# Kernel tuning notes

Hardware: AMD Instinct MI355X
Metric: run time of the kernel (lower is better)

## Reference

```python
import jax, jax.numpy as jnp
import numpy as np

D_MODEL = 2048
NUM_HEADS = 16
D_K = D_MODEL // NUM_HEADS
THETA = 10000.0
MAX_SEQ_LEN = 2048
GPT_INIT_STD = 0.02


def setup_inputs() -> dict:
    key = jax.random.key(0)
    ks = jax.random.split(key, 5)
    B, T = 4, 2048
    x = jax.random.normal(ks[0], (B, T, D_MODEL), dtype=jnp.float32)
    token_positions = jnp.arange(T, dtype=jnp.int64 if jax.config.jax_enable_x64 else jnp.int32)[None, :]
    Wq = jax.random.normal(ks[1], (D_MODEL, D_MODEL), dtype=jnp.float32) * GPT_INIT_STD
    Wk = jax.random.normal(ks[2], (D_MODEL, D_MODEL), dtype=jnp.float32) * GPT_INIT_STD
    Wv = jax.random.normal(ks[3], (D_MODEL, D_MODEL), dtype=jnp.float32) * GPT_INIT_STD
    Wo = jax.random.normal(ks[4], (D_MODEL, D_MODEL), dtype=jnp.float32) * GPT_INIT_STD
    return {"x": x, "token_positions": token_positions, "Wq": Wq, "Wk": Wk, "Wv": Wv, "Wo": Wo}


def _rope_tables(dtype):
    # angles[p, j] = p * theta^(-2j/d_k), j in [0, d_k/2)
    j = jnp.arange(D_K // 2, dtype=jnp.float32)
    inv_freq = THETA ** (-2.0 * j / float(D_K))
    pos = jnp.arange(MAX_SEQ_LEN, dtype=jnp.float32)[:, None]
    angles = pos * inv_freq[None, :]
    return jnp.cos(angles).astype(dtype), jnp.sin(angles).astype(dtype)


def _apply_rope(t, cos_pos, sin_pos):
    # t: (b, h, s, d); cos/sin: (1, s, d/2) -> broadcast over (b, h)
    even = t[..., 0::2]
    odd = t[..., 1::2]
    c = cos_pos[:, None, :, :]  # (1,1,s,d/2)
    s = sin_pos[:, None, :, :]
    rot_even = even * c - odd * s
    rot_odd = even * s + odd * c
    out = jnp.stack([rot_even, rot_odd], axis=-1)  # (b,h,s,d/2,2)
    return out.reshape(t.shape)


def reference(x, token_positions, Wq, Wk, Wv, Wo):
    B, T, D = x.shape
    H, d = NUM_HEADS, D_K
    q = (x @ Wq.T).reshape(B, T, H, d).transpose(0, 2, 1, 3)  # (b,h,t,d)
    k = (x @ Wk.T).reshape(B, T, H, d).transpose(0, 2, 1, 3)
    v = (x @ Wv.T).reshape(B, T, H, d).transpose(0, 2, 1, 3)

    cos_tab, sin_tab = _rope_tables(x.dtype)
    cos_pos = cos_tab[token_positions]  # (1, t, d/2)
    sin_pos = sin_tab[token_positions]
    q = _apply_rope(q, cos_pos, sin_pos)
    k = _apply_rope(k, cos_pos, sin_pos)

    # token_positions is strictly increasing and attention_mask is None,
    # so build_attention_mask returns None -> unmasked eager attention.
    scale = float(d) ** -0.5
    scores = jnp.einsum('bhtd,bhsd->bhts', q, k) * scale
    attn = jax.nn.softmax(scores.astype(jnp.float32), axis=-1).astype(q.dtype)
    out = jnp.einsum('bhts,bhsd->bhtd', attn, v)  # (b,h,t,d)
    out = out.transpose(0, 2, 1, 3).reshape(B, T, D)  # (b,t,h*d)
    return out @ Wo.T
```

## Files before the change

kernel.cpp:

```cpp
#include <hip/hip_runtime.h>
#include <hip/hip_bf16.h>
#include <hip/hip_fp16.h>
#include <math.h>

#define TSEQ   2048
#define DMODEL 2048
#define NHEAD  16
#define DHEAD  128
#define NBATCH 4
#define MROWS  (NBATCH*TSEQ)

typedef __attribute__((ext_vector_type(8))) short v8s;
typedef __attribute__((ext_vector_type(4))) float v4f;
typedef __attribute__((ext_vector_type(16))) float v16f;

#if __has_builtin(__builtin_amdgcn_exp2f)
#define EXP2(x) __builtin_amdgcn_exp2f(x)
#else
#define EXP2(x) __expf((x) * 0.6931471805599453f)
#endif

__device__ __forceinline__ unsigned short f2b(float f) {
  __hip_bfloat16 h = __float2bfloat16(f);
  return *reinterpret_cast<unsigned short*>(&h);
}
__device__ __forceinline__ float b2f(unsigned int u) {
  unsigned short us = (unsigned short)u;
  __hip_bfloat16 h = *reinterpret_cast<__hip_bfloat16*>(&us);
  return __bfloat162float(h);
}
__device__ __forceinline__ unsigned int cvtpk(float lo, float hi) {
  unsigned int r;
  asm("v_cvt_pk_bf16_f32 %0, %1, %2" : "=v"(r) : "v"(lo), "v"(hi));
  return r;
}
__device__ __forceinline__ void gload_lds16(const unsigned short* g, unsigned short* l) {
  __builtin_amdgcn_global_load_lds(
      (const __attribute__((address_space(1))) unsigned int*)g,
      (__attribute__((address_space(3))) unsigned int*)l, 16, 0, 0);
}

__global__ void prep_kernel(const float* __restrict__ x,  const float* __restrict__ Wq,
                            const float* __restrict__ Wk, const float* __restrict__ Wv,
                            const float* __restrict__ Wo, const int* __restrict__ pos,
                            unsigned short* __restrict__ xb,  unsigned short* __restrict__ wqb,
                            unsigned short* __restrict__ wkb, unsigned short* __restrict__ wvb,
                            unsigned short* __restrict__ wob,
                            unsigned int* __restrict__ ropeT) {
  const int blk = blockIdx.x, tid = threadIdx.x;
  if (blk < 32768) {
    const float* in; unsigned short* out; int lb;
    if      (blk < 16384) { in = x;  out = xb;  lb = blk; }
    else if (blk < 20480) { in = Wq; out = wqb; lb = blk - 16384; }
    else if (blk < 24576) { in = Wk; out = wkb; lb = blk - 20480; }
    else if (blk < 28672) { in = Wv; out = wvb; lb = blk - 24576; }
    else                  { in = Wo; out = wob; lb = blk - 28672; }
    int i = lb * 256 + tid;
    float4 v = reinterpret_cast<const float4*>(in)[i];
    ushort4 o;
    o.x = f2b(v.x); o.y = f2b(v.y); o.z = f2b(v.z); o.w = f2b(v.w);
    reinterpret_cast<ushort4*>(out)[i] = o;
  } else {
    int idx = (blk - 32768) * 256 + tid;
    int t = idx >> 6, j = idx & 63;
    float p = (float)pos[t];
    float inv_freq = expf((-2.0f * (float)j / 128.0f) * logf(10000.0f));
    float ang = p * inv_freq;
    __half2 h2 = __floats2half2_rn(cosf(ang), sinf(ang));
    ropeT[idx] = *reinterpret_cast<unsigned int*>(&h2);
  }
}

template<int MODE>
__global__ __launch_bounds__(512, 2) void gemm8(const unsigned short* __restrict__ A,
                                                const unsigned short* __restrict__ Bt,
                                                void* __restrict__ Cout,
                                                const unsigned int* __restrict__ ropeT) {
  __shared__ unsigned short SL[65536];
  const int tid = threadIdx.x;
  const int lane = tid & 63, wv = tid >> 6;
  const int wr = wv >> 2, wc = wv & 3;
  const int g = lane >> 4, r16 = lane & 15;
  const int r7 = r16 & 7;
  const int sl0 = (g ^ r7) << 3;
  const int sl1 = ((4 + g) ^ r7) << 3;

  const int nx = gridDim.x;
  const int nwg = nx * gridDim.y;
  const int lid = blockIdx.y * nx + blockIdx.x;
  const int q8 = nwg >> 3, r8 = nwg & 7;
  const int xcd = lid & 7, off = lid >> 3;
  const int nlid = (xcd < r8 ? xcd * (q8 + 1) : r8 * (q8 + 1) + (xcd - r8) * q8) + off;
  const int mrow0 = (nlid / nx) * 256;
  const int ncol0 = (nlid % nx) * 256;

  const int srow = tid >> 3;
  const int sslot = tid & 7;

  auto stA = [&](int kt, int b, int hf) {
    const int k0 = kt * 64;
#pragma unroll
    for (int j = 0; j < 2; ++j) {
      int r = hf * 128 + j * 64 + srow;
      int slot = sslot ^ (r & 7);
      gload_lds16(&A[(size_t)(mrow0 + r) * DMODEL + k0 + slot * 8],
                  &SL[b * 16384 + (hf * 128 + j * 64) * 64 + tid * 8]);
    }
  };
  auto stB = [&](int kt, int b, int hf) {
    const int k0 = kt * 64;
#pragma unroll
    for (int j = 0; j < 2; ++j) {
      int r = hf * 128 + j * 64 + srow;
      int slot = sslot ^ (r & 7);
      gload_lds16(&Bt[(size_t)(ncol0 + r) * DMODEL + k0 + slot * 8],
                  &SL[32768 + b * 16384 + (hf * 128 + j * 64) * 64 + tid * 8]);
    }
  };

  v4f zero = {0.f, 0.f, 0.f, 0.f};
  v4f acc[8][4];
#pragma unroll
  for (int m = 0; m < 8; ++m)
#pragma unroll
    for (int n = 0; n < 4; ++n) acc[m][n] = zero;

  stA(0, 0, 0); stA(0, 0, 1); stB(0, 0, 0); stB(0, 0, 1);
  stA(1, 1, 0); stA(1, 1, 1); stB(1, 1, 0); stB(1, 1, 1);
  asm volatile("s_waitcnt vmcnt(8)" ::: "memory");
  __builtin_amdgcn_s_barrier();

  v8s af[4][2], bf[4][2];
  const int arow = wr * 128 + r16;
  const int brow = wc * 64 + r16;

  for (int kt = 0; kt < DMODEL / 64; ++kt) {
    const int p = kt & 1;
    unsigned short* LA = SL + p * 16384;
    unsigned short* LB = SL + 32768 + p * 16384;

#pragma unroll
    for (int m = 0; m < 4; ++m) {
      af[m][0] = *(const v8s*)&LA[(arow + m * 16) * 64 + sl0];
      af[m][1] = *(const v8s*)&LA[(arow + m * 16) * 64 + sl1];
    }
#pragma unroll
    for (int n = 0; n < 2; ++n) {
      bf[n][0] = *(const v8s*)&LB[(brow + n * 16) * 64 + sl0];
      bf[n][1] = *(const v8s*)&LB[(brow + n * 16) * 64 + sl1];
    }
    __builtin_amdgcn_s_barrier();
    asm volatile("s_waitcnt lgkmcnt(0)" ::: "memory");
    __builtin_amdgcn_sched_barrier(0);
    __builtin_amdgcn_s_setprio(1);
#pragma unroll
    for (int m = 0; m < 4; ++m)
#pragma unroll
      for (int n = 0; n < 2; ++n) {
        acc[m][n] = __builtin_amdgcn_mfma_f32_16x16x32_bf16(af[m][0], bf[n][0], acc[m][n], 0, 0, 0);
        acc[m][n] = __builtin_amdgcn_mfma_f32_16x16x32_bf16(af[m][1], bf[n][1], acc[m][n], 0, 0, 0);
      }
    __builtin_amdgcn_s_setprio(0);
    __builtin_amdgcn_s_barrier();

#pragma unroll
    for (int n = 2; n < 4; ++n) {
      bf[n][0] = *(const v8s*)&LB[(brow + n * 16) * 64 + sl0];
      bf[n][1] = *(const v8s*)&LB[(brow + n * 16) * 64 + sl1];
    }
    __builtin_amdgcn_s_barrier();
    asm volatile("s_waitcnt lgkmcnt(0)" ::: "memory");
    __builtin_amdgcn_sched_barrier(0);
    __builtin_amdgcn_s_setprio(1);
#pragma unroll
    for (int m = 0; m < 4; ++m)
#pragma unroll
      for (int n = 2; n < 4; ++n) {
        acc[m][n] = __builtin_amdgcn_mfma_f32_16x16x32_bf16(af[m][0], bf[n][0], acc[m][n], 0, 0, 0);
        acc[m][n] = __builtin_amdgcn_mfma_f32_16x16x32_bf16(af[m][1], bf[n][1], acc[m][n], 0, 0, 0);
      }
    __builtin_amdgcn_s_setprio(0);
    __builtin_amdgcn_s_barrier();

#pragma unroll
    for (int m = 0; m < 4; ++m) {
      af[m][0] = *(const v8s*)&LA[(arow + 64 + m * 16) * 64 + sl0];
      af[m][1] = *(const v8s*)&LA[(arow + 64 + m * 16) * 64 + sl1];
    }
    if (kt < DMODEL / 64 - 2) { stB(kt + 2, p, 0); stB(kt + 2, p, 1); }
    __builtin_amdgcn_s_barrier();
    asm volatile("s_waitcnt lgkmcnt(0)" ::: "memory");
    __builtin_amdgcn_sched_barrier(0);
    __builtin_amdgcn_s_setprio(1);
#pragma unroll
    for (int m = 0; m < 4; ++m)
#pragma unroll
      for (int n = 2; n < 4; ++n) {
        acc[m + 4][n] = __builtin_amdgcn_mfma_f32_16x16x32_bf16(af[m][0], bf[n][0], acc[m + 4][n], 0, 0, 0);
        acc[m + 4][n] = __builtin_amdgcn_mfma_f32_16x16x32_bf16(af[m][1], bf[n][1], acc[m + 4][n], 0, 0, 0);
      }
    __builtin_amdgcn_s_setprio(0);
    __builtin_amdgcn_s_barrier();

    if (kt < DMODEL / 64 - 2) {
      stA(kt + 2, p, 0); stA(kt + 2, p, 1);
      asm volatile("s_waitcnt vmcnt(8)" ::: "memory");
    } else {
      asm volatile("s_waitcnt vmcnt(0)" ::: "memory");
    }
    __builtin_amdgcn_s_barrier();
    __builtin_amdgcn_s_setprio(1);
#pragma unroll
    for (int m = 0; m < 4; ++m)
#pragma unroll
      for (int n = 0; n < 2; ++n) {
        acc[m + 4][n] = __builtin_amdgcn_mfma_f32_16x16x32_bf16(af[m][0], bf[n][0], acc[m + 4][n], 0, 0, 0);
        acc[m + 4][n] = __builtin_amdgcn_mfma_f32_16x16x32_bf16(af[m][1], bf[n][1], acc[m + 4][n], 0, 0, 0);
      }
    __builtin_amdgcn_s_setprio(0);
    __builtin_amdgcn_s_barrier();
  }

  if (MODE <= 1) {
    unsigned short* reg = SL + wv * 4608;
    const int band = ncol0 + wc * 64;
    const int h2 = band >> 7;
    const int dd0 = band & 127;
    const int lr2b = lane >> 2, c4 = lane & 3;
    const float SC = 0.12751726f;
#pragma unroll
    for (int hf = 0; hf < 2; ++hf) {
#pragma unroll
      for (int m = 0; m < 4; ++m)
#pragma unroll
        for (int n = 0; n < 4; ++n)
#pragma unroll
          for (int r = 0; r < 4; ++r)
            reg[(m * 16 + g * 4 + r) * 72 + n * 16 + r16] = f2b(acc[hf * 4 + m][n][r]);
      asm volatile("s_waitcnt lgkmcnt(0)" ::: "memory");
      __builtin_amdgcn_sched_barrier(0);
#pragma unroll
      for (int ps = 0; ps < 4; ++ps) {
        int lr2 = ps * 16 + lr2b;
        v8s d0 = *(const v8s*)&reg[lr2 * 72 + c4 * 16];
        v8s d1 = *(const v8s*)&reg[lr2 * 72 + c4 * 16 + 8];
        int row = mrow0 + wr * 128 + hf * 64 + lr2;
        int t = row & (TSEQ - 1), bb = row >> 11;
        const uint4* tp = (const uint4*)&ropeT[(t << 6) + (dd0 >> 1) + c4 * 8];
        uint4 t0 = tp[0], t1 = tp[1];
        unsigned int ow[8];
#pragma unroll
        for (int k = 0; k < 8; ++k) {
          unsigned int cs = (k < 4) ? (&t0.x)[k] : (&t1.x)[k - 4];
          __half2 hcs = *reinterpret_cast<__half2*>(&cs);
          float c = __half2float(__low2half(hcs));
          float s = __half2float(__high2half(hcs));
          int kk = (k & 3) * 2;
          float e = (k < 4) ? b2f((unsigned short)d0[kk])     : b2f((unsigned short)d1[kk]);
          float o = (k < 4) ? b2f((unsigned short)d0[kk + 1]) : b2f((unsigned short)d1[kk + 1]);
          float re = e * c - o * s;
          float ro = e * s + o * c;
          if (MODE == 0) { re *= SC; ro *= SC; }
          ow[k] = cvtpk(re, ro);
        }
        unsigned short* dst = (unsigned short*)Cout +
            (((size_t)bb * NHEAD + h2) * TSEQ + t) * DHEAD + dd0 + c4 * 16;
        *(uint4*)dst = make_uint4(ow[0], ow[1], ow[2], ow[3]);
        *(uint4*)(dst + 8) = make_uint4(ow[4], ow[5], ow[6], ow[7]);
      }
      if (hf == 0) {
        asm volatile("s_waitcnt lgkmcnt(0)" ::: "memory");
        __builtin_amdgcn_sched_barrier(0);
      }
    }
  } else {
#pragma unroll
    for (int m = 0; m < 8; ++m) {
#pragma unroll
      for (int n = 0; n < 4; ++n) {
#pragma unroll
        for (int r = 0; r < 4; ++r) {
          int row = mrow0 + wr * 128 + m * 16 + g * 4 + r;
          int col = ncol0 + wc * 64 + n * 16 + r16;
          float val = acc[m][n][r];
          if (MODE == 2) {
            int hh = row >> 7, dd = row & (DHEAD - 1);
            int bb = col >> 11, tt = col & (TSEQ - 1);
            ((unsigned short*)Cout)[(((size_t)bb * NHEAD + hh) * DHEAD + dd) * TSEQ + tt] = f2b(val);
          } else {
            ((float*)Cout)[(size_t)row * DMODEL + col] = val;
          }
        }
      }
    }
  }
}

__global__ __launch_bounds__(256, 2) void attn_kernel(const unsigned short* __restrict__ Q,
                                                      const unsigned short* __restrict__ K,
                                                      const unsigned short* __restrict__ Vt,
                                                      unsigned short* __restrict__ O) {
  __shared__ unsigned short Ks[64 * 128];
  __shared__ unsigned short Vs[64 * 128];
  const int tid = threadIdx.x, lane = tid & 63, w = tid >> 6;
  const int hi = lane >> 5, l31 = lane & 31;
  const int bh = blockIdx.y;
  const int b = bh >> 4, h = bh & 15;
  const int qbase = blockIdx.x * 128;
  const size_t hb = (size_t)bh * TSEQ * DHEAD;
  const size_t vb = (size_t)bh * DHEAD * TSEQ;

  v8s qf[8];
  {
    const int qrow = qbase + w * 32 + l31;
#pragma unroll
    for (int dk = 0; dk < 8; ++dk)
      qf[dk] = *(const v8s*)&Q[hb + (size_t)qrow * DHEAD + dk * 16 + hi * 8];
  }

  v16f Z16 = {0,0,0,0,0,0,0,0,0,0,0,0,0,0,0,0};
  v16f o_acc[4];
#pragma unroll
  for (int d = 0; d < 4; ++d) o_acc[d] = Z16;
  float l_run = 0.0f;

  const int ck0 = tid;
  v8s kst[4], vst[4];

#pragma unroll
  for (int hh = 0; hh < 4; ++hh) {
    int ck = ck0 + hh * 256;
    kst[hh] = *(const v8s*)&K[hb + (size_t)(ck >> 4) * DHEAD + (ck & 15) * 8];
    vst[hh] = *(const v8s*)&Vt[vb + (size_t)(ck >> 3) * TSEQ + (ck & 7) * 8];
  }
#pragma unroll
  for (int hh = 0; hh < 4; ++hh) {
    int ck = ck0 + hh * 256;
    int kr = ck >> 4, kc = (ck & 15) * 8;
    *(v8s*)&Ks[kr * 128 + (kc ^ ((kr & 15) << 3))] = kst[hh];
    int vr = ck >> 3, vg = ck & 7;
    int slot = (((vr & 1) << 3) | vg) ^ ((vr >> 1) & 15);
    *(v8s*)&Vs[(vr >> 1) * 128 + slot * 8] = vst[hh];
  }
  __syncthreads();

  for (int s0 = 0; s0 < TSEQ; s0 += 64) {
    const bool last = (s0 + 64 >= TSEQ);
    if (!last) {
#pragma unroll
      for (int hh = 0; hh < 4; ++hh) {
        int ck = ck0 + hh * 256;
        kst[hh] = *(const v8s*)&K[hb + (size_t)(s0 + 64 + (ck >> 4)) * DHEAD + (ck & 15) * 8];
      }
#pragma unroll
      for (int hh = 0; hh < 4; ++hh) {
        int ck = ck0 + hh * 256;
        vst[hh] = *(const v8s*)&Vt[vb + (size_t)(ck >> 3) * TSEQ + s0 + 64 + (ck & 7) * 8];
      }
    }

    v16f s[2]; s[0] = Z16; s[1] = Z16;
    __builtin_amdgcn_s_setprio(1);
#pragma unroll
    for (int kvt = 0; kvt < 2; ++kvt) {
#pragma unroll
      for (int dk = 0; dk < 8; ++dk) {
        int krow = kvt * 32 + l31;
        v8s a = *(const v8s*)&Ks[krow * 128 + ((dk * 16 + hi * 8) ^ ((krow & 15) << 3))];
        s[kvt] = __builtin_amdgcn_mfma_f32_32x32x16_bf16(a, qf[dk], s[kvt], 0, 0, 0);
      }
    }
    __builtin_amdgcn_s_setprio(0);

    __syncthreads();

    if (!last) {
#pragma unroll
      for (int hh = 0; hh < 4; ++hh) {
        int ck = ck0 + hh * 256;
        int kr = ck >> 4, kc = (ck & 15) * 8;
        *(v8s*)&Ks[kr * 128 + (kc ^ ((kr & 15) << 3))] = kst[hh];
      }
    }

    float rowsum = 0.f;
#pragma unroll
    for (int kvt = 0; kvt < 2; ++kvt)
#pragma unroll
      for (int r = 0; r < 16; ++r) {
        float pp = EXP2(s[kvt][r]);
        s[kvt][r] = pp; rowsum += pp;
      }
    l_run += rowsum;

    union { unsigned int u[4]; v8s v; } pf[4];
#pragma unroll
    for (int kvt = 0; kvt < 2; ++kvt) {
      unsigned int wpk[8];
#pragma unroll
      for (int i = 0; i < 8; ++i) wpk[i] = cvtpk(s[kvt][2 * i], s[kvt][2 * i + 1]);
      asm("v_permlane32_swap_b32 %0, %1" : "+v"(wpk[0]), "+v"(wpk[2]));
      asm("v_permlane32_swap_b32 %0, %1" : "+v"(wpk[1]), "+v"(wpk[3]));
      asm("v_permlane32_swap_b32 %0, %1" : "+v"(wpk[4]), "+v"(wpk[6]));
      asm("v_permlane32_swap_b32 %0, %1" : "+v"(wpk[5]), "+v"(wpk[7]));
      pf[2 * kvt].u[0] = wpk[0]; pf[2 * kvt].u[1] = wpk[1];
      pf[2 * kvt].u[2] = wpk[2]; pf[2 * kvt].u[3] = wpk[3];
      pf[2 * kvt + 1].u[0] = wpk[4]; pf[2 * kvt + 1].u[1] = wpk[5];
      pf[2 * kvt + 1].u[2] = wpk[6]; pf[2 * kvt + 1].u[3] = wpk[7];
    }

    __builtin_amdgcn_s_setprio(1);
#pragma unroll
    for (int kvt = 0; kvt < 2; ++kvt) {
      const int g0 = kvt * 4 + hi;
#pragma unroll
      for (int d = 0; d < 4; ++d) {
        int drow = d * 32 + l31;
        int lr = drow >> 1;
        int x = (drow & 1) << 3;
        int sw = lr & 15;
        v8s vf0 = *(const v8s*)&Vs[lr * 128 + (((x | g0) ^ sw) << 3)];
        v8s vf1 = *(const v8s*)&Vs[lr * 128 + (((x | (g0 + 2)) ^ sw) << 3)];
        o_acc[d] = __builtin_amdgcn_mfma_f32_32x32x16_bf16(pf[2 * kvt].v, vf0, o_acc[d], 0, 0, 0);
        o_acc[d] = __builtin_amdgcn_mfma_f32_32x32x16_bf16(pf[2 * kvt + 1].v, vf1, o_acc[d], 0, 0, 0);
      }
    }
    __builtin_amdgcn_s_setprio(0);

    __syncthreads();

    if (!last) {
#pragma unroll
      for (int hh = 0; hh < 4; ++hh) {
        int ck = ck0 + hh * 256;
        int vr = ck >> 3, vg = ck & 7;
        int slot = (((vr & 1) << 3) | vg) ^ ((vr >> 1) & 15);
        *(v8s*)&Vs[(vr >> 1) * 128 + slot * 8] = vst[hh];
      }
    }
  }

#pragma unroll
  for (int r = 0; r < 16; ++r) {
    int qi = (r & 3) + 8 * (r >> 2) + 4 * hi;
    float lq = __shfl(l_run, qi) + __shfl(l_run, qi + 32);
    float inv = 1.0f / lq;
    int t = qbase + w * 32 + qi;
#pragma unroll
    for (int d = 0; d < 4; ++d) {
      O[((size_t)(b * TSEQ + t)) * DMODEL + h * DHEAD + d * 32 + l31] = f2b(o_acc[d][r] * inv);
    }
  }
}

extern "C" void kernel_launch(void* const* d_in, const int* in_sizes, int n_in,
                              void* d_out, int out_size, void* d_ws, size_t ws_size,
                              hipStream_t stream) {
  const float* x  = (const float*)d_in[0];
  const int*   pos = (const int*)d_in[1];
  const float* Wq = (const float*)d_in[2];
  const float* Wk = (const float*)d_in[3];
  const float* Wv = (const float*)d_in[4];
  const float* Wo = (const float*)d_in[5];
  float* out = (float*)d_out;
  char* ws = (char*)d_ws;

  const size_t WBYTES = (size_t)DMODEL * DMODEL * 2;
  const size_t XBYTES = (size_t)MROWS * DMODEL * 2;
  unsigned short* wqb = (unsigned short*)(ws);
  unsigned short* wkb = (unsigned short*)(ws + WBYTES);
  unsigned short* wvb = (unsigned short*)(ws + 2 * WBYTES);
  unsigned short* wob = (unsigned short*)(ws + 3 * WBYTES);
  unsigned short* xb  = (unsigned short*)(ws + 4 * WBYTES);
  unsigned short* Qb  = (unsigned short*)(ws + 4 * WBYTES + XBYTES);
  unsigned short* Kb  = (unsigned short*)(ws + 4 * WBYTES + 2 * XBYTES);
  unsigned short* Vtb = (unsigned short*)(ws + 4 * WBYTES + 3 * XBYTES);
  unsigned int* ropeT = (unsigned int*)(ws + 4 * WBYTES + 4 * XBYTES);
  if (ws_size < 4 * WBYTES + 4 * XBYTES + (size_t)TSEQ * 64 * sizeof(unsigned int)) return;

  prep_kernel<<<33280, 256, 0, stream>>>(x, Wq, Wk, Wv, Wo, pos,
                                         xb, wqb, wkb, wvb, wob, ropeT);

  dim3 gg(DMODEL / 256, MROWS / 256);
  gemm8<0><<<gg, 512, 0, stream>>>(xb, wqb, (void*)Qb, ropeT);
  gemm8<1><<<gg, 512, 0, stream>>>(xb, wkb, (void*)Kb, ropeT);
  gemm8<2><<<dim3(MROWS / 256, DMODEL / 256), 512, 0, stream>>>(wvb, xb, (void*)Vtb, ropeT);

  attn_kernel<<<dim3(TSEQ / 128, 64), 256, 0, stream>>>(Qb, Kb, Vtb, xb);

  gemm8<3><<<gg, 512, 0, stream>>>(xb, wob, (void*)out, ropeT);
}
```

Measured before the change: 467.3 us.

## Double-buffer attention K/V via direct global-to-LDS loads, two Q tiles per wave

The attention kernel now stages K and V into double-buffered LDS using direct global-to-LDS loads, with the swizzle moved into the source addresses. This replaces the register-staged copy and the two barriers per iteration with one waitcnt plus barrier. Each wave now handles 64 query rows (two 32-row tiles), so each K/V fragment read from LDS feeds twice as many MFMAs, and the grid is halved. The trade-offs are higher register pressure, double the LDS footprint and fewer blocks, which may reduce occupancy. The kernel also depends on a gload_lds16 helper assumed to be defined in the unseen part of the file.

```diff
diff --git a/kernel.cpp b/kernel.cpp
--- a/kernel.cpp
+++ b/kernel.cpp
@@ -300,118 +300,103 @@
                                                       const unsigned short* __restrict__ K,
                                                       const unsigned short* __restrict__ Vt,
                                                       unsigned short* __restrict__ O) {
-  __shared__ unsigned short Ks[64 * 128];
-  __shared__ unsigned short Vs[64 * 128];
+  __shared__ unsigned short Ks[2][64 * 128];
+  __shared__ unsigned short Vs[2][64 * 128];
   const int tid = threadIdx.x, lane = tid & 63, w = tid >> 6;
   const int hi = lane >> 5, l31 = lane & 31;
   const int bh = blockIdx.y;
   const int b = bh >> 4, h = bh & 15;
-  const int qbase = blockIdx.x * 128;
+  const int qbase = blockIdx.x * 256;
   const size_t hb = (size_t)bh * TSEQ * DHEAD;
   const size_t vb = (size_t)bh * DHEAD * TSEQ;
 
-  v8s qf[8];
+  v8s qf0[8], qf1[8];
   {
-    const int qrow = qbase + w * 32 + l31;
-#pragma unroll
-    for (int dk = 0; dk < 8; ++dk)
-      qf[dk] = *(const v8s*)&Q[hb + (size_t)qrow * DHEAD + dk * 16 + hi * 8];
+    const int qr0 = qbase + w * 64 + l31;
+#pragma unroll
+    for (int dk = 0; dk < 8; ++dk) {
+      qf0[dk] = *(const v8s*)&Q[hb + (size_t)qr0 * DHEAD + dk * 16 + hi * 8];
+      qf1[dk] = *(const v8s*)&Q[hb + (size_t)(qr0 + 32) * DHEAD + dk * 16 + hi * 8];
+    }
   }
 
   v16f Z16 = {0,0,0,0,0,0,0,0,0,0,0,0,0,0,0,0};
-  v16f o_acc[4];
-#pragma unroll
-  for (int d = 0; d < 4; ++d) o_acc[d] = Z16;
-  float l_run = 0.0f;
-
-  const int ck0 = tid;
-  v8s kst[4], vst[4];
-
-#pragma unroll
-  for (int hh = 0; hh < 4; ++hh) {
-    int ck = ck0 + hh * 256;
-    kst[hh] = *(const v8s*)&K[hb + (size_t)(ck >> 4) * DHEAD + (ck & 15) * 8];
-    vst[hh] = *(const v8s*)&Vt[vb + (size_t)(ck >> 3) * TSEQ + (ck & 7) * 8];
-  }
-#pragma unroll
-  for (int hh = 0; hh < 4; ++hh) {
-    int ck = ck0 + hh * 256;
-    int kr = ck >> 4, kc = (ck & 15) * 8;
-    *(v8s*)&Ks[kr * 128 + (kc ^ ((kr & 15) << 3))] = kst[hh];
-    int vr = ck >> 3, vg = ck & 7;
-    int slot = (((vr & 1) << 3) | vg) ^ ((vr >> 1) & 15);
-    *(v8s*)&Vs[(vr >> 1) * 128 + slot * 8] = vst[hh];
-  }
-  __syncthreads();
-
-  for (int s0 = 0; s0 < TSEQ; s0 += 64) {
-    const bool last = (s0 + 64 >= TSEQ);
-    if (!last) {
-#pragma unroll
-      for (int hh = 0; hh < 4; ++hh) {
-        int ck = ck0 + hh * 256;
-        kst[hh] = *(const v8s*)&K[hb + (size_t)(s0 + 64 + (ck >> 4)) * DHEAD + (ck & 15) * 8];
-      }
-#pragma unroll
-      for (int hh = 0; hh < 4; ++hh) {
-        int ck = ck0 + hh * 256;
-        vst[hh] = *(const v8s*)&Vt[vb + (size_t)(ck >> 3) * TSEQ + s0 + 64 + (ck & 7) * 8];
-      }
-    }
-
-    v16f s[2]; s[0] = Z16; s[1] = Z16;
-    __builtin_amdgcn_s_setprio(1);
+  v16f o0[4], o1[4];
+#pragma unroll
+  for (int d = 0; d < 4; ++d) { o0[d] = Z16; o1[d] = Z16; }
+  float l0 = 0.0f, l1 = 0.0f;
+
+  const unsigned short* ksrc;
+  const unsigned short* vsrc;
+  {
+    int kr = tid >> 4, kc = (tid & 15) ^ (kr & 15);
+    ksrc = K + hb + (size_t)kr * DHEAD + kc * 8;
+    int lr = tid >> 4, sp = (tid & 15) ^ (lr & 15);
+    int vr = 2 * lr + (sp >> 3), vg = sp & 7;
+    vsrc = Vt + vb + (size_t)vr * TSEQ + vg * 8;
+  }
+  auto stage = [&](const unsigned short* kp, const unsigned short* vp, int buf) {
+#pragma unroll
+    for (int j = 0; j < 4; ++j) {
+      gload_lds16(kp + (size_t)j * 16 * DHEAD, &Ks[buf][(j * 256 + tid) * 8]);
+      gload_lds16(vp + (size_t)j * 32 * TSEQ, &Vs[buf][(j * 256 + tid) * 8]);
+    }
+  };
+
+  stage(ksrc, vsrc, 0);
+  asm volatile("s_waitcnt vmcnt(0)" ::: "memory");
+  __builtin_amdgcn_s_barrier();
+
+  for (int t = 0; t < TSEQ / 64; ++t) {
+    const int p = t & 1;
+    if (t < TSEQ / 64 - 1)
+      stage(ksrc + (size_t)(t + 1) * 64 * DHEAD, vsrc + (size_t)(t + 1) * 64, p ^ 1);
+
+    float rs0 = 0.f, rs1 = 0.f;
 #pragma unroll
     for (int kvt = 0; kvt < 2; ++kvt) {
+      v16f s0 = Z16, s1 = Z16;
+      __builtin_amdgcn_s_setprio(1);
 #pragma unroll
       for (int dk = 0; dk < 8; ++dk) {
         int krow = kvt * 32 + l31;
-        v8s a = *(const v8s*)&Ks[krow * 128 + ((dk * 16 + hi * 8) ^ ((krow & 15) << 3))];
-        s[kvt] = __builtin_amdgcn_mfma_f32_32x32x16_bf16(a, qf[dk], s[kvt], 0, 0, 0);
-      }
-    }
-    __builtin_amdgcn_s_setprio(0);
-
-    __syncthreads();
-
-    if (!last) {
-#pragma unroll
-      for (int hh = 0; hh < 4; ++hh) {
-        int ck = ck0 + hh * 256;
-        int kr = ck >> 4, kc = (ck & 15) * 8;
-        *(v8s*)&Ks[kr * 128 + (kc ^ ((kr & 15) << 3))] = kst[hh];
-      }
-    }
-
-    float rowsum = 0.f;
-#pragma unroll
-    for (int kvt = 0; kvt < 2; ++kvt)
+        v8s a = *(const v8s*)&Ks[p][krow * 128 + ((dk * 16 + hi * 8) ^ ((krow & 15) << 3))];
+        s0 = __builtin_amdgcn_mfma_f32_32x32x16_bf16(a, qf0[dk], s0, 0, 0, 0);
+        s1 = __builtin_amdgcn_mfma_f32_32x32x16_bf16(a, qf1[dk], s1, 0, 0, 0);
+      }
+      __builtin_amdgcn_s_setprio(0);
+
 #pragma unroll
       for (int r = 0; r < 16; ++r) {
-        float pp = EXP2(s[kvt][r]);
-        s[kvt][r] = pp; rowsum += pp;
-      }
-    l_run += rowsum;
-
-    union { unsigned int u[4]; v8s v; } pf[4];
-#pragma unroll
-    for (int kvt = 0; kvt < 2; ++kvt) {
-      unsigned int wpk[8];
-#pragma unroll
-      for (int i = 0; i < 8; ++i) wpk[i] = cvtpk(s[kvt][2 * i], s[kvt][2 * i + 1]);
-      asm("v_permlane32_swap_b32 %0, %1" : "+v"(wpk[0]), "+v"(wpk[2]));
-      asm("v_permlane32_swap_b32 %0, %1" : "+v"(wpk[1]), "+v"(wpk[3]));
-      asm("v_permlane32_swap_b32 %0, %1" : "+v"(wpk[4]), "+v"(wpk[6]));
-      asm("v_permlane32_swap_b32 %0, %1" : "+v"(wpk[5]), "+v"(wpk[7]));
-      pf[2 * kvt].u[0] = wpk[0]; pf[2 * kvt].u[1] = wpk[1];
-      pf[2 * kvt].u[2] = wpk[2]; pf[2 * kvt].u[3] = wpk[3];
-      pf[2 * kvt + 1].u[0] = wpk[4]; pf[2 * kvt + 1].u[1] = wpk[5];
-      pf[2 * kvt + 1].u[2] = wpk[6]; pf[2 * kvt + 1].u[3] = wpk[7];
-    }
-
-    __builtin_amdgcn_s_setprio(1);
-#pragma unroll
-    for (int kvt = 0; kvt < 2; ++kvt) {
+        float p0 = EXP2(s0[r]); s0[r] = p0; rs0 += p0;
+        float p1 = EXP2(s1[r]); s1[r] = p1; rs1 += p1;
+      }
+
+      union { unsigned int u[4]; v8s v; } pa0, pb0, pa1, pb1;
+      {
+        unsigned int wk[8];
+#pragma unroll
+        for (int i = 0; i < 8; ++i) wk[i] = cvtpk(s0[2 * i], s0[2 * i + 1]);
+        asm("v_permlane32_swap_b32 %0, %1" : "+v"(wk[0]), "+v"(wk[2]));
+        asm("v_permlane32_swap_b32 %0, %1" : "+v"(wk[1]), "+v"(wk[3]));
+        asm("v_permlane32_swap_b32 %0, %1" : "+v"(wk[4]), "+v"(wk[6]));
+        asm("v_permlane32_swap_b32 %0, %1" : "+v"(wk[5]), "+v"(wk[7]));
+        pa0.u[0] = wk[0]; pa0.u[1] = wk[1]; pa0.u[2] = wk[2]; pa0.u[3] = wk[3];
+        pb0.u[0] = wk[4]; pb0.u[1] = wk[5]; pb0.u[2] = wk[6]; pb0.u[3] = wk[7];
+      }
+      {
+        unsigned int wk[8];
+#pragma unroll
+        for (int i = 0; i < 8; ++i) wk[i] = cvtpk(s1[2 * i], s1[2 * i + 1]);
+        asm("v_permlane32_swap_b32 %0, %1" : "+v"(wk[0]), "+v"(wk[2]));
+        asm("v_permlane32_swap_b32 %0, %1" : "+v"(wk[1]), "+v"(wk[3]));
+        asm("v_permlane32_swap_b32 %0, %1" : "+v"(wk[4]), "+v"(wk[6]));
+        asm("v_permlane32_swap_b32 %0, %1" : "+v"(wk[5]), "+v"(wk[7]));
+        pa1.u[0] = wk[0]; pa1.u[1] = wk[1]; pa1.u[2] = wk[2]; pa1.u[3] = wk[3];
+        pb1.u[0] = wk[4]; pb1.u[1] = wk[5]; pb1.u[2] = wk[6]; pb1.u[3] = wk[7];
+      }
+
+      __builtin_amdgcn_s_setprio(1);
       const int g0 = kvt * 4 + hi;
 #pragma unroll
       for (int d = 0; d < 4; ++d) {
@@ -419,36 +404,32 @@
         int lr = drow >> 1;
         int x = (drow & 1) << 3;
         int sw = lr & 15;
-        v8s vf0 = *(const v8s*)&Vs[lr * 128 + (((x | g0) ^ sw) << 3)];
-        v8s vf1 = *(const v8s*)&Vs[lr * 128 + (((x | (g0 + 2)) ^ sw) << 3)];
-        o_acc[d] = __builtin_amdgcn_mfma_f32_32x32x16_bf16(pf[2 * kvt].v, vf0, o_acc[d], 0, 0, 0);
-        o_acc[d] = __builtin_amdgcn_mfma_f32_32x32x16_bf16(pf[2 * kvt + 1].v, vf1, o_acc[d], 0, 0, 0);
-      }
-    }
-    __builtin_amdgcn_s_setprio(0);
-
-    __syncthreads();
-
-    if (!last) {
-#pragma unroll
-      for (int hh = 0; hh < 4; ++hh) {
-        int ck = ck0 + hh * 256;
-        int vr = ck >> 3, vg = ck & 7;
-        int slot = (((vr & 1) << 3) | vg) ^ ((vr >> 1) & 15);
-        *(v8s*)&Vs[(vr >> 1) * 128 + slot * 8] = vst[hh];
-      }
-    }
+        v8s vf0 = *(const v8s*)&Vs[p][lr * 128 + (((x | g0) ^ sw) << 3)];
+        v8s vf1 = *(const v8s*)&Vs[p][lr * 128 + (((x | (g0 + 2)) ^ sw) << 3)];
+        o0[d] = __builtin_amdgcn_mfma_f32_32x32x16_bf16(pa0.v, vf0, o0[d], 0, 0, 0);
+        o0[d] = __builtin_amdgcn_mfma_f32_32x32x16_bf16(pb0.v, vf1, o0[d], 0, 0, 0);
+        o1[d] = __builtin_amdgcn_mfma_f32_32x32x16_bf16(pa1.v, vf0, o1[d], 0, 0, 0);
+        o1[d] = __builtin_amdgcn_mfma_f32_32x32x16_bf16(pb1.v, vf1, o1[d], 0, 0, 0);
+      }
+      __builtin_amdgcn_s_setprio(0);
+    }
+    l0 += rs0; l1 += rs1;
+
+    asm volatile("s_waitcnt vmcnt(0)" ::: "memory");
+    __builtin_amdgcn_s_barrier();
   }
 
 #pragma unroll
   for (int r = 0; r < 16; ++r) {
     int qi = (r & 3) + 8 * (r >> 2) + 4 * hi;
-    float lq = __shfl(l_run, qi) + __shfl(l_run, qi + 32);
-    float inv = 1.0f / lq;
-    int t = qbase + w * 32 + qi;
+    float lq0 = __shfl(l0, qi) + __shfl(l0, qi + 32);
+    float lq1 = __shfl(l1, qi) + __shfl(l1, qi + 32);
+    float i0 = 1.0f / lq0, i1 = 1.0f / lq1;
+    int t0 = qbase + w * 64 + qi;
 #pragma unroll
     for (int d = 0; d < 4; ++d) {
-      O[((size_t)(b * TSEQ + t)) * DMODEL + h * DHEAD + d * 32 + l31] = f2b(o_acc[d][r] * inv);
+      O[((size_t)(b * TSEQ + t0)) * DMODEL + h * DHEAD + d * 32 + l31] = f2b(o0[d][r] * i0);
+      O[((size_t)(b * TSEQ + t0 + 32)) * DMODEL + h * DHEAD + d * 32 + l31] = f2b(o1[d][r] * i1);
     }
   }
 }
@@ -486,7 +467,7 @@
   gemm8<1><<<gg, 512, 0, stream>>>(xb, wkb, (void*)Kb, ropeT);
   gemm8<2><<<dim3(MROWS / 256, DMODEL / 256), 512, 0, stream>>>(wvb, xb, (void*)Vtb, ropeT);
 
-  attn_kernel<<<dim3(TSEQ / 128, 64), 256, 0, stream>>>(Qb, Kb, Vtb, xb);
+  attn_kernel<<<dim3(TSEQ / 256, 64), 256, 0, stream>>>(Qb, Kb, Vtb, xb);
 
   gemm8<3><<<gg, 512, 0, stream>>>(xb, wob, (void*)out, ropeT);
 }
```

New measurement: 470.1 us. Within noise of the previous version (+0.6%).
